# Kernel tuning notes

Hardware: AMD Instinct MI355X
Metric: run time of the kernel (lower is better)

## Reference

```python
import jax, jax.numpy as jnp
import numpy as np

IN_SIZE = 1024
HIDDEN = 1024
BATCH = 4096


def _linear_params(key, out_dim, in_dim):
    # torch nn.Linear init: U(-1/sqrt(in_dim), 1/sqrt(in_dim)) for W and b
    k1, k2 = jax.random.split(key)
    bound = 1.0 / np.sqrt(in_dim)
    W = jax.random.uniform(k1, (out_dim, in_dim), jnp.float32, -bound, bound)
    b = jax.random.uniform(k2, (out_dim,), jnp.float32, -bound, bound)
    return W, b


def setup_inputs() -> dict:
    key = jax.random.key(0)
    keys = jax.random.split(key, 11)
    x = jax.random.normal(keys[0], (BATCH, IN_SIZE), jnp.float32)
    hidden = jax.random.normal(keys[1], (BATCH, HIDDEN), jnp.float32)
    cell = jax.random.normal(keys[2], (BATCH, HIDDEN), jnp.float32)
    names = ['xf', 'xi', 'xo', 'xc', 'hf', 'hi', 'ho', 'hc']
    inp = {'x': x, 'hidden': hidden, 'cell': cell}
    for n, k in zip(names, keys[3:]):
        in_dim = IN_SIZE if n[0] == 'x' else HIDDEN
        W, b = _linear_params(k, HIDDEN, in_dim)
        inp['W_' + n] = W
        inp['b_' + n] = b
    return inp


def reference(x, hidden, cell,
              W_xf, b_xf, W_xi, b_xi, W_xo, b_xo, W_xc, b_xc,
              W_hf, b_hf, W_hi, b_hi, W_ho, b_ho, W_hc, b_hc):
    # gates: sigmoid/tanh over (x-linear + h-linear) pairs
    f = jax.nn.sigmoid(x @ W_xf.T + b_xf + hidden @ W_hf.T + b_hf)
    i = jax.nn.sigmoid(x @ W_xi.T + b_xi + hidden @ W_hi.T + b_hi)
    o = jax.nn.sigmoid(x @ W_xo.T + b_xo + hidden @ W_ho.T + b_ho)
    c = jnp.tanh(x @ W_xc.T + b_xc + hidden @ W_hc.T + b_hc)
    updated_cell = f * cell + i * c
    updated_hidden = o * jnp.tanh(updated_cell)
    return updated_hidden, updated_cell
```

## Files before the change

kernel.cpp:

```cpp
#include <hip/hip_runtime.h>
#include <hip/hip_bf16.h>

#define BATCH 4096
#define NH    1024
#define KCAT  2048
#define NJ    4096
#define NT    (KCAT / 64)
#define NIT   (NT / 2)

typedef __bf16 bf16x8 __attribute__((ext_vector_type(8)));
typedef float  f32x4  __attribute__((ext_vector_type(4)));
typedef unsigned short u16x8 __attribute__((ext_vector_type(8)));

struct WPtrs { const float* wx[4]; const float* wh[4]; };
struct BPtrs { const float* bx[4]; const float* bh[4]; };

__device__ __forceinline__ unsigned short f2b(float f) {
  union { float f; unsigned u; } v; v.f = f;
  return (unsigned short)((v.u + 0x7fffu + ((v.u >> 16) & 1u)) >> 16);
}

__device__ __forceinline__ void gload_lds16(const void* g, void* l) {
  __builtin_amdgcn_global_load_lds(
      (const __attribute__((address_space(1))) unsigned int*)g,
      (__attribute__((address_space(3))) unsigned int*)l, 16, 0, 0);
}

__device__ __forceinline__ float sigmoid_f(float x) {
  x = fminf(fmaxf(x, -30.f), 30.f);
  return 1.f / (1.f + __expf(-x));
}
__device__ __forceinline__ float tanh_f(float x) {
  x = fminf(fmaxf(x, -15.f), 15.f);
  float e = __expf(2.f * x);
  return (e - 1.f) / (e + 1.f);
}

__global__ __launch_bounds__(256) void pack_all(
    const float* __restrict__ x, const float* __restrict__ h,
    WPtrs W, BPtrs B,
    __hip_bfloat16* __restrict__ Acat, __hip_bfloat16* __restrict__ Bcat,
    float* __restrict__ biasc) {
  int bid = blockIdx.x;
  if (bid < 4096) {
    int t = bid * 256 + threadIdx.x;
    int base = t * 8;
    int row = base >> 11;
    int k   = base & 2047;
    const float* src = (k < 1024) ? (x + (size_t)row * 1024 + k)
                                  : (h + (size_t)row * 1024 + (k - 1024));
    float4 v0 = ((const float4*)src)[0];
    float4 v1 = ((const float4*)src)[1];
    u16x8 o;
    o[0]=f2b(v0.x); o[1]=f2b(v0.y); o[2]=f2b(v0.z); o[3]=f2b(v0.w);
    o[4]=f2b(v1.x); o[5]=f2b(v1.y); o[6]=f2b(v1.z); o[7]=f2b(v1.w);
    *(u16x8*)((unsigned short*)Acat + base) = o;
  } else if (bid < 8192) {
    int t = (bid - 4096) * 256 + threadIdx.x;
    int base = t * 8;
    int j = base >> 11;
    int k = base & 2047;
    int n = ((j >> 6) << 4) + (j & 15);
    int g = (j >> 4) & 3;
    const float* src = (k < 1024) ? (W.wx[g] + (size_t)n * 1024 + k)
                                  : (W.wh[g] + (size_t)n * 1024 + (k - 1024));
    float4 v0 = ((const float4*)src)[0];
    float4 v1 = ((const float4*)src)[1];
    u16x8 o;
    o[0]=f2b(v0.x); o[1]=f2b(v0.y); o[2]=f2b(v0.z); o[3]=f2b(v0.w);
    o[4]=f2b(v1.x); o[5]=f2b(v1.y); o[6]=f2b(v1.z); o[7]=f2b(v1.w);
    *(u16x8*)((unsigned short*)Bcat + base) = o;
  } else {
    int i = (bid - 8192) * 256 + threadIdx.x;
    int g = i >> 10, n = i & 1023;
    biasc[i] = B.bx[g][n] + B.bh[g][n];
  }
}


#define STAGE_A_HALF(T, H)                                                      \
  {                                                                             \
    _Pragma("unroll")                                                           \
    for (int i_ = 0; i_ < 2; ++i_) {                                            \
      gload_lds16(Ag + (size_t)((H)*128 + i_*64 + strow) * KCAT + (T)*64 +      \
                      stchnk * 8,                                               \
                  &smem[((T)&1)*32768 + (H)*8192 + i_*4096 + w*512]);           \
    }                                                                           \
  }
#define STAGE_B_HALF(T, H)                                                      \
  {                                                                             \
    _Pragma("unroll")                                                           \
    for (int i_ = 0; i_ < 2; ++i_) {                                            \
      gload_lds16(Bg + (size_t)((H)*128 + i_*64 + strow) * KCAT + (T)*64 +      \
                      stchnk * 8,                                               \
                  &smem[((T)&1)*32768 + 16384 + (H)*8192 + i_*4096 + w*512]);   \
    }                                                                           \
  }

#define READ_A(BUFO, MQ)                                                        \
  {                                                                             \
    _Pragma("unroll")                                                           \
    for (int mf_ = 0; mf_ < 4; ++mf_) {                                         \
      af[mf_][0] = *(const bf16x8*)(smc + (BUFO) + arow0 +                      \
                                    ((MQ)*4 + mf_)*2048 + colb0);               \
      af[mf_][1] = *(const bf16x8*)(smc + (BUFO) + arow0 +                      \
                                    ((MQ)*4 + mf_)*2048 + colb1);               \
    }                                                                           \
  }
#define READ_B(BUFO, NQ)                                                        \
  {                                                                             \
    _Pragma("unroll")                                                           \
    for (int nf_ = 0; nf_ < 2; ++nf_) {                                         \
      bfr[NQ][nf_][0] = *(const bf16x8*)(smc + (BUFO) + brow0 +                 \
                                         ((NQ)*2 + nf_)*2048 + colb0);          \
      bfr[NQ][nf_][1] = *(const bf16x8*)(smc + (BUFO) + brow0 +                 \
                                         ((NQ)*2 + nf_)*2048 + colb1);          \
    }                                                                           \
  }
#define MFMA_Q(MQ, NQ)                                                          \
  {                                                                             \
    _Pragma("unroll")                                                           \
    for (int ks_ = 0; ks_ < 2; ++ks_)                                           \
      _Pragma("unroll")                                                         \
      for (int mf_ = 0; mf_ < 4; ++mf_)                                         \
        _Pragma("unroll")                                                       \
        for (int nf_ = 0; nf_ < 2; ++nf_)                                       \
          acc[(MQ)*4 + mf_][(NQ)*2 + nf_] =                                     \
              __builtin_amdgcn_mfma_f32_16x16x32_bf16(                          \
                  af[mf_][ks_], bfr[NQ][nf_][ks_],                              \
                  acc[(MQ)*4 + mf_][(NQ)*2 + nf_], 0, 0, 0);                    \
  }

#define BAR    __builtin_amdgcn_s_barrier()
#define LGKM0  { asm volatile("s_waitcnt lgkmcnt(0)" ::: "memory");             \
                 __builtin_amdgcn_sched_barrier(0); }
#define LGKM8  asm volatile("s_waitcnt lgkmcnt(8)" ::: "memory")
#define PRIO1  __builtin_amdgcn_s_setprio(1)
#define PRIO0  __builtin_amdgcn_s_setprio(0)

__global__ __launch_bounds__(512, 2) void lstm_gemm8(
    const unsigned short* __restrict__ Acat,
    const unsigned short* __restrict__ Bcat,
    const float* __restrict__ biasc,
    const float* __restrict__ cell,
    float* __restrict__ outH, float* __restrict__ outC) {
  __shared__ unsigned short smem[65536];

  const int tid  = threadIdx.x;
  const int w    = tid >> 6;
  const int lane = tid & 63;
  const int wr   = w >> 2;
  const int wc   = w & 3;
  const int lr   = lane & 15;
  const int cb0  = ((lane >> 4) & 3) * 16;
  const int sx   = (lr & 7) << 4;

  const int bid = blockIdx.x;
  const int s   = (bid & 7) * 32 + (bid >> 3);
  const int bx  = s & 15;
  const int by  = s >> 4;

  const unsigned short* Ag = Acat + (size_t)(by * 256) * KCAT;
  const unsigned short* Bg = Bcat + (size_t)(bx * 256) * KCAT;

  const int strow  = w * 8 + (lane >> 3);
  const int stchnk = (lane & 7) ^ ((lane >> 3) & 7);

  const int arow0 = (wr * 128 + lr) * 128;
  const int brow0 = 32768 + (wc * 64 + lr) * 128;
  const int colb0 = cb0 ^ sx;
  const int colb1 = (64 + cb0) ^ sx;
  const char* smc = (const char*)smem;

  f32x4 acc[8][4] = {};
  bf16x8 af[4][2];
  bf16x8 bfr[2][2][2];

  STAGE_A_HALF(0, 0);
  STAGE_A_HALF(0, 1);
  STAGE_B_HALF(0, 0);
  STAGE_B_HALF(0, 1);
  STAGE_B_HALF(1, 0);
  STAGE_B_HALF(1, 1);
  asm volatile("s_waitcnt vmcnt(4)" ::: "memory");
  __builtin_amdgcn_sched_barrier(0);
  BAR;

  for (int it = 0; it < NIT; ++it) {
    const int t0 = 2 * it;
    const bool full = (t0 + 2 < NT);

    READ_A(0, 0);
    READ_B(0, 0);
    STAGE_A_HALF(t0 + 1, 0);
    LGKM8;
    BAR; LGKM0;
    PRIO1; MFMA_Q(0, 0); PRIO0;
    BAR;
    READ_B(0, 1);
    STAGE_A_HALF(t0 + 1, 1);
    BAR; LGKM0;
    PRIO1; MFMA_Q(0, 1); PRIO0;
    BAR;
    READ_A(0, 1);
    if (full) STAGE_B_HALF(t0 + 2, 0);
    BAR; LGKM0;
    PRIO1; MFMA_Q(1, 0); PRIO0;
    BAR;
    if (full) {
      STAGE_B_HALF(t0 + 2, 1);
      asm volatile("s_waitcnt vmcnt(4)" ::: "memory");
    } else {
      asm volatile("s_waitcnt vmcnt(0)" ::: "memory");
    }
    __builtin_amdgcn_sched_barrier(0);
    BAR; LGKM0;
    PRIO1; MFMA_Q(1, 1); PRIO0;
    BAR;

    READ_A(65536, 0);
    READ_B(65536, 0);
    if (full) STAGE_A_HALF(t0 + 2, 0);
    LGKM8;
    BAR; LGKM0;
    PRIO1; MFMA_Q(0, 0); PRIO0;
    BAR;
    READ_B(65536, 1);
    if (full) STAGE_A_HALF(t0 + 2, 1);
    BAR; LGKM0;
    PRIO1; MFMA_Q(0, 1); PRIO0;
    BAR;
    READ_A(65536, 1);
    if (full) STAGE_B_HALF(t0 + 3, 0);
    BAR; LGKM0;
    PRIO1; MFMA_Q(1, 0); PRIO0;
    BAR;
    if (full) {
      STAGE_B_HALF(t0 + 3, 1);
      asm volatile("s_waitcnt vmcnt(4)" ::: "memory");
      __builtin_amdgcn_sched_barrier(0);
    }
    BAR; LGKM0;
    PRIO1; MFMA_Q(1, 1); PRIO0;
    BAR;
  }

  const int n_out = (bx * 4 + wc) * 16 + lr;
  const float bfv = biasc[n_out];
  const float biv = biasc[1024 + n_out];
  const float bov = biasc[2048 + n_out];
  const float bcv = biasc[3072 + n_out];
  const int q0 = (lane >> 4) * 4;

#pragma unroll
  for (int m = 0; m < 8; ++m) {
    int row0 = by * 256 + wr * 128 + m * 16 + q0;
#pragma unroll
    for (int q = 0; q < 4; ++q) {
      int row = row0 + q;
      float pf = acc[m][0][q] + bfv;
      float pi = acc[m][1][q] + biv;
      float po = acc[m][2][q] + bov;
      float pc = acc[m][3][q] + bcv;
      float fg = sigmoid_f(pf);
      float ig = sigmoid_f(pi);
      float og = sigmoid_f(po);
      float cg = tanh_f(pc);
      float cold = cell[(size_t)row * NH + n_out];
      float cn = fg * cold + ig * cg;
      float hn = og * tanh_f(cn);
      outH[(size_t)row * NH + n_out] = hn;
      outC[(size_t)row * NH + n_out] = cn;
    }
  }
}

extern "C" void kernel_launch(void* const* d_in, const int* in_sizes, int n_in,
                              void* d_out, int out_size, void* d_ws, size_t ws_size,
                              hipStream_t stream) {
  const float* x    = (const float*)d_in[0];
  const float* h    = (const float*)d_in[1];
  const float* cell = (const float*)d_in[2];
  WPtrs wp; BPtrs bp;
  for (int g = 0; g < 4; ++g) {
    wp.wx[g] = (const float*)d_in[3 + 2 * g];
    bp.bx[g] = (const float*)d_in[4 + 2 * g];
    wp.wh[g] = (const float*)d_in[11 + 2 * g];
    bp.bh[g] = (const float*)d_in[12 + 2 * g];
  }

  char* ws = (char*)d_ws;
  __hip_bfloat16* Acat = (__hip_bfloat16*)ws;
  __hip_bfloat16* Bcat = (__hip_bfloat16*)(ws + (size_t)BATCH * KCAT * 2);
  float* biasc = (float*)(ws + (size_t)BATCH * KCAT * 2 + (size_t)NJ * KCAT * 2);

  float* outH = (float*)d_out;
  float* outC = outH + (size_t)BATCH * NH;

  pack_all<<<8208, 256, 0, stream>>>(x, h, wp, bp, Acat, Bcat, biasc);

  lstm_gemm8<<<256, 512, 0, stream>>>((const unsigned short*)Acat,
                                      (const unsigned short*)Bcat,
                                      biasc, cell, outH, outC);
}
```

Baseline: 85.69 us.

## Software-pipeline LDS fragment reads to overlap with MFMA in single-tile loop

Restructures the main GEMM loop from a manually unrolled two-tile body into a single-tile loop where LDS reads for the next quadrant or next tile are issued before or alongside the current MFMA block. This uses double-buffered B fragment registers. Explicit lgkmcnt waits and sched_barriers are removed, and roughly one barrier per quadrant is dropped, leaving wait placement to the compiler. The aim is to hide LDS read latency behind MFMA work. The trade-off is higher register pressure and less explicit control over instruction scheduling.

```diff
diff --git a/kernel.cpp b/kernel.cpp
--- a/kernel.cpp
+++ b/kernel.cpp
@@ -6,7 +6,6 @@
 #define KCAT  2048
 #define NJ    4096
 #define NT    (KCAT / 64)
-#define NIT   (NT / 2)
 
 typedef __bf16 bf16x8 __attribute__((ext_vector_type(8)));
 typedef float  f32x4  __attribute__((ext_vector_type(4)));
@@ -107,17 +106,17 @@
                                     ((MQ)*4 + mf_)*2048 + colb1);               \
     }                                                                           \
   }
-#define READ_B(BUFO, NQ)                                                        \
+#define READ_B(BUFO, NQ, DST)                                                   \
   {                                                                             \
     _Pragma("unroll")                                                           \
     for (int nf_ = 0; nf_ < 2; ++nf_) {                                         \
-      bfr[NQ][nf_][0] = *(const bf16x8*)(smc + (BUFO) + brow0 +                 \
-                                         ((NQ)*2 + nf_)*2048 + colb0);          \
-      bfr[NQ][nf_][1] = *(const bf16x8*)(smc + (BUFO) + brow0 +                 \
-                                         ((NQ)*2 + nf_)*2048 + colb1);          \
-    }                                                                           \
-  }
-#define MFMA_Q(MQ, NQ)                                                          \
+      DST[nf_][0] = *(const bf16x8*)(smc + (BUFO) + brow0 +                     \
+                                     ((NQ)*2 + nf_)*2048 + colb0);              \
+      DST[nf_][1] = *(const bf16x8*)(smc + (BUFO) + brow0 +                     \
+                                     ((NQ)*2 + nf_)*2048 + colb1);              \
+    }                                                                           \
+  }
+#define MFMA_Q(MQ, NQ, BSET)                                                    \
   {                                                                             \
     _Pragma("unroll")                                                           \
     for (int ks_ = 0; ks_ < 2; ++ks_)                                           \
@@ -127,14 +126,11 @@
         for (int nf_ = 0; nf_ < 2; ++nf_)                                       \
           acc[(MQ)*4 + mf_][(NQ)*2 + nf_] =                                     \
               __builtin_amdgcn_mfma_f32_16x16x32_bf16(                          \
-                  af[mf_][ks_], bfr[NQ][nf_][ks_],                              \
+                  af[mf_][ks_], BSET[nf_][ks_],                                 \
                   acc[(MQ)*4 + mf_][(NQ)*2 + nf_], 0, 0, 0);                    \
   }
 
 #define BAR    __builtin_amdgcn_s_barrier()
-#define LGKM0  { asm volatile("s_waitcnt lgkmcnt(0)" ::: "memory");             \
-                 __builtin_amdgcn_sched_barrier(0); }
-#define LGKM8  asm volatile("s_waitcnt lgkmcnt(8)" ::: "memory")
 #define PRIO1  __builtin_amdgcn_s_setprio(1)
 #define PRIO0  __builtin_amdgcn_s_setprio(0)
 
@@ -174,7 +170,8 @@
 
   f32x4 acc[8][4] = {};
   bf16x8 af[4][2];
-  bf16x8 bfr[2][2][2];
+  bf16x8 bfr0[2][2];
+  bf16x8 bfr1[2][2];
 
   STAGE_A_HALF(0, 0);
   STAGE_A_HALF(0, 1);
@@ -183,66 +180,39 @@
   STAGE_B_HALF(1, 0);
   STAGE_B_HALF(1, 1);
   asm volatile("s_waitcnt vmcnt(4)" ::: "memory");
-  __builtin_amdgcn_sched_barrier(0);
   BAR;
-
-  for (int it = 0; it < NIT; ++it) {
-    const int t0 = 2 * it;
-    const bool full = (t0 + 2 < NT);
-
-    READ_A(0, 0);
-    READ_B(0, 0);
-    STAGE_A_HALF(t0 + 1, 0);
-    LGKM8;
-    BAR; LGKM0;
-    PRIO1; MFMA_Q(0, 0); PRIO0;
-    BAR;
-    READ_B(0, 1);
-    STAGE_A_HALF(t0 + 1, 1);
-    BAR; LGKM0;
-    PRIO1; MFMA_Q(0, 1); PRIO0;
-    BAR;
-    READ_A(0, 1);
-    if (full) STAGE_B_HALF(t0 + 2, 0);
-    BAR; LGKM0;
-    PRIO1; MFMA_Q(1, 0); PRIO0;
-    BAR;
-    if (full) {
-      STAGE_B_HALF(t0 + 2, 1);
+  READ_A(0, 0);
+  READ_B(0, 0, bfr0);
+
+  for (int t = 0; t < NT; ++t) {
+    const int curo = (t & 1) * 65536;
+    const int nxto = curo ^ 65536;
+    const bool s1 = (t + 1 < NT);
+    const bool s2 = (t + 2 < NT);
+
+    BAR;
+    if (s1) STAGE_A_HALF(t + 1, 0);
+    PRIO1; MFMA_Q(0, 0, bfr0); PRIO0;
+    READ_B(curo, 1, bfr1);
+    BAR;
+    if (s1) STAGE_A_HALF(t + 1, 1);
+    PRIO1; MFMA_Q(0, 1, bfr1); PRIO0;
+    READ_A(curo, 1);
+    BAR;
+    if (s2) STAGE_B_HALF(t + 2, 0);
+    PRIO1; MFMA_Q(1, 0, bfr0); PRIO0;
+    if (s2) {
+      STAGE_B_HALF(t + 2, 1);
       asm volatile("s_waitcnt vmcnt(4)" ::: "memory");
-    } else {
+    } else if (s1) {
       asm volatile("s_waitcnt vmcnt(0)" ::: "memory");
     }
-    __builtin_amdgcn_sched_barrier(0);
-    BAR; LGKM0;
-    PRIO1; MFMA_Q(1, 1); PRIO0;
-    BAR;
-
-    READ_A(65536, 0);
-    READ_B(65536, 0);
-    if (full) STAGE_A_HALF(t0 + 2, 0);
-    LGKM8;
-    BAR; LGKM0;
-    PRIO1; MFMA_Q(0, 0); PRIO0;
-    BAR;
-    READ_B(65536, 1);
-    if (full) STAGE_A_HALF(t0 + 2, 1);
-    BAR; LGKM0;
-    PRIO1; MFMA_Q(0, 1); PRIO0;
-    BAR;
-    READ_A(65536, 1);
-    if (full) STAGE_B_HALF(t0 + 3, 0);
-    BAR; LGKM0;
-    PRIO1; MFMA_Q(1, 0); PRIO0;
-    BAR;
-    if (full) {
-      STAGE_B_HALF(t0 + 3, 1);
-      asm volatile("s_waitcnt vmcnt(4)" ::: "memory");
-      __builtin_amdgcn_sched_barrier(0);
+    BAR;
+    PRIO1; MFMA_Q(1, 1, bfr1); PRIO0;
+    if (s1) {
+      READ_A(nxto, 0);
+      READ_B(nxto, 0, bfr0);
     }
-    BAR; LGKM0;
-    PRIO1; MFMA_Q(1, 1); PRIO0;
-    BAR;
   }
 
   const int n_out = (bx * 4 + wc) * 16 + lr;
```

Result: no change. 84.33 us (median of 3 runs) (-1.6%).
